# Performance work log

Hardware: AMD Instinct MI355X
Metric: run time of the kernel (lower is better)

## Reference

```python
import jax, jax.numpy as jnp
import numpy as np

K = 16  # k1: neighbors kept
D = 2   # d1: dilation


def setup_inputs() -> dict:
    key = jax.random.key(0)
    k1, k2 = jax.random.split(key)
    new_xyz = jax.random.normal(k1, (8, 4096, 3), dtype=jnp.float32)
    new_points = jax.random.normal(k2, (8, 4096, 64), dtype=jnp.float32)
    return {"new_xyz": new_xyz, "new_points": new_points}


def _dg_knn_idx(new_points):
    sq = jnp.sum(new_points * new_points, axis=-1)              # [B,N]
    inner = jnp.einsum('bnc,bmc->bnm', new_points, new_points)  # [B,N,N]
    adj = sq[:, :, None] - 2.0 * inner + sq[:, None, :]
    # dilated kNN: top (K*D) nearest, then stride by D
    _, idx = jax.lax.top_k(-adj, K * D)                         # [B,N,K*D]
    return idx[:, :, ::D]                                       # [B,N,K]


def reference(new_xyz, new_points):
    nn_idx = _dg_knn_idx(new_points)                            # [B,N,K] int32
    # index_points: gather neighbor coordinates -> [B,N,K,3]
    neighbor_xyz = jax.vmap(lambda pts, idx: pts[idx])(new_xyz, nn_idx)
    xyz_tile = jnp.broadcast_to(new_xyz[:, :, None, :], neighbor_xyz.shape)
    relative_xyz = xyz_tile - neighbor_xyz                      # [B,N,K,3]
    relative_dis = jnp.sqrt(jnp.sum(relative_xyz * relative_xyz, axis=-1, keepdims=True))
    # [B,N,K, 1+3+3+3] = [B,N,K,10]
    return jnp.concatenate([relative_dis, relative_xyz, xyz_tile, neighbor_xyz], axis=-1)
```

## Files before the change

### kernel.cpp

```cpp
#include <hip/hip_runtime.h>
#include <stdint.h>

typedef unsigned long long u64;
typedef __attribute__((ext_vector_type(8))) short s16x8;
typedef __attribute__((ext_vector_type(4))) float f32x4v;
typedef __attribute__((ext_vector_type(4))) unsigned int u32x4;
typedef __attribute__((ext_vector_type(2))) unsigned int u32x2;

#define NB 8
#define NPTS 4096
#define NC 64
#define KOUT 16
#define TSEL 48
#define CHUNK 64
#define NCHUNK (NPTS / CHUNK)
#define IDXBITS 0xFFFu
#define KEYMASK 0xFFFFF000u
#define RPW 4
#define RPB 16
#define ROWB 144

__global__ __launch_bounds__(256) void sq_kernel(const float* __restrict__ pts,
                                                 float* __restrict__ sqw) {
    int p = blockIdx.x * 256 + threadIdx.x;
    const float* r = pts + (size_t)p * NC;
    float acc[8];
#pragma unroll
    for (int j = 0; j < 8; ++j) acc[j] = __fmul_rn(r[j], r[j]);
#pragma unroll
    for (int i = 8; i < 64; i += 8)
#pragma unroll
        for (int j = 0; j < 8; ++j)
            acc[j] = __fadd_rn(acc[j], __fmul_rn(r[i + j], r[i + j]));
    float s01 = __fadd_rn(acc[0], acc[1]);
    float s23 = __fadd_rn(acc[2], acc[3]);
    float s45 = __fadd_rn(acc[4], acc[5]);
    float s67 = __fadd_rn(acc[6], acc[7]);
    sqw[p] = __fadd_rn(__fadd_rn(s01, s23), __fadd_rn(s45, s67));
}

static __device__ __forceinline__ uint32_t pkbf(float a, float b) {
#if __has_builtin(__builtin_amdgcn_perm)
    return __builtin_amdgcn_perm(__float_as_uint(b), __float_as_uint(a), 0x07060302);
#else
    return (__float_as_uint(b) & 0xFFFF0000u) | (__float_as_uint(a) >> 16);
#endif
}

__device__ __forceinline__ void stream_insert(uint32_t& list, uint32_t cand, int lane) {
    uint32_t thr = (uint32_t)__builtin_amdgcn_readlane((int)list, 47);
    u64 mask = __ballot(cand < thr);
    while (mask) {
        int src = __ffsll((long long)mask) - 1;
        uint32_t v = (uint32_t)__builtin_amdgcn_readlane((int)cand, src);
        int pos = __popcll(__ballot(list < v));
        uint32_t up = __shfl_up(list, 1);
        list = (lane < pos) ? list : ((lane == pos) ? v : up);
        mask &= (mask - 1);
    }
}

__device__ __forceinline__ void epilogue(uint32_t list, int n, int b, int lane,
                                         const float* __restrict__ pb,
                                         const float* __restrict__ sqb,
                                         float sqn,
                                         const float* __restrict__ xyz,
                                         float* __restrict__ out) {
    int m = (int)(list & IDXBITS);
    const float4* xr = (const float4*)(pb + (size_t)n * NC);
    const float4* yr = (const float4*)(pb + (size_t)m * NC);
    float acc = 0.f;
#pragma unroll
    for (int i = 0; i < 16; ++i) {
        float4 xv = xr[i];
        float4 yv = yr[i];
        acc = __fmaf_rn(xv.x, yv.x, acc);
        acc = __fmaf_rn(xv.y, yv.y, acc);
        acc = __fmaf_rn(xv.z, yv.z, acc);
        acc = __fmaf_rn(xv.w, yv.w, acc);
    }
    float key = __fadd_rn(__fsub_rn(sqn, __fmul_rn(2.0f, acc)), sqb[m]);

    int rank = 0;
    uint32_t kb = __float_as_uint(key);
#pragma unroll 1
    for (int j = 0; j < TSEL; ++j) {
        float kj = __uint_as_float(
            (uint32_t)__builtin_amdgcn_readlane((int)kb, j));
        int mj = __builtin_amdgcn_readlane(m, j);
        bool less = (kj < key) || (kj == key && mj < m);
        rank += less ? 1 : 0;
    }
    if (lane < TSEL && rank < 2 * KOUT && (rank & 1) == 0) {
        int k = rank >> 1;
        const float* xn = xyz + ((size_t)b * NPTS + n) * 3;
        const float* xm = xyz + ((size_t)b * NPTS + m) * 3;
        float xnx = xn[0], xny = xn[1], xnz = xn[2];
        float ox = xm[0], oy = xm[1], oz = xm[2];
        float rx = xnx - ox, ry = xny - oy, rz = xnz - oz;
        float dis = sqrtf(rx * rx + ry * ry + rz * rz);
        float* o = out + (((size_t)b * NPTS + n) * KOUT + k) * 10;
        o[0] = dis; o[1] = rx; o[2] = ry; o[3] = rz;
        o[4] = xnx; o[5] = xny; o[6] = xnz;
        o[7] = ox;  o[8] = oy;  o[9] = oz;
    }
}

__global__ __launch_bounds__(256, 3) void knn_kernel(
    const float* __restrict__ xyz,
    const float* __restrict__ pts,
    const float* __restrict__ sqw,
    float* __restrict__ out) {

    __shared__ __align__(16) unsigned short ylds[2][CHUNK * (ROWB / 2)];
    __shared__ __align__(16) float slds[4][16][20];

    const int tid = threadIdx.x;
    const int lane = tid & 63;
    const int wave = tid >> 6;
    const int b = blockIdx.x >> 8;
    const int rowbase = (blockIdx.x & 255) << 4;
    const int nw = __builtin_amdgcn_readfirstlane(rowbase + wave * RPW);
    const float* pb = pts + (size_t)b * NPTS * NC;
    const float* sqb = sqw + (size_t)b * NPTS;

    s16x8 afrag0, afrag1;
    {
        const float* xrow = pb + (size_t)(rowbase + (lane & 15)) * NC + (lane >> 4) * 8;
        float4 xa0 = *(const float4*)(xrow);
        float4 xa1 = *(const float4*)(xrow + 4);
        float4 xb0 = *(const float4*)(xrow + 32);
        float4 xb1 = *(const float4*)(xrow + 36);
        u32x4 a0p = { pkbf(xa0.x, xa0.y), pkbf(xa0.z, xa0.w),
                      pkbf(xa1.x, xa1.y), pkbf(xa1.z, xa1.w) };
        u32x4 a1p = { pkbf(xb0.x, xb0.y), pkbf(xb0.z, xb0.w),
                      pkbf(xb1.x, xb1.y), pkbf(xb1.z, xb1.w) };
        afrag0 = __builtin_bit_cast(s16x8, a0p);
        afrag1 = __builtin_bit_cast(s16x8, a1p);
    }

    const float sqn0 = sqb[nw + 0];
    const float sqn1 = sqb[nw + 1];
    const float sqn2 = sqb[nw + 2];
    const float sqn3 = sqb[nw + 3];

    uint32_t list0 = 0xFFFFFFFFu, list1 = 0xFFFFFFFFu;
    uint32_t list2 = 0xFFFFFFFFu, list3 = 0xFFFFFFFFu;

    const float4* gsrc = (const float4*)pb;
    float4 pf[4];
#pragma unroll
    for (int j = 0; j < 4; ++j) pf[j] = gsrc[tid + 256 * j];

#pragma unroll
    for (int j = 0; j < 4; ++j) {
        int s = tid + 256 * j;
        u32x2 w2 = { pkbf(pf[j].x, pf[j].y), pkbf(pf[j].z, pf[j].w) };
        *(u32x2*)((char*)ylds[0] + (s >> 4) * ROWB + (s & 15) * 8) = w2;
    }
    __syncthreads();

    for (int c = 0; c < NCHUNK; ++c) {
        const int cb = c & 1;
        if (c + 1 < NCHUNK) {
#pragma unroll
            for (int j = 0; j < 4; ++j)
                pf[j] = gsrc[(size_t)(c + 1) * (CHUNK * 16) + tid + 256 * j];
        }
        {
            const int m = c * CHUNK + lane;
            float sqm = sqb[m];
            const char* bp = (const char*)ylds[cb] + wave * (16 * ROWB)
                           + (lane & 15) * ROWB + (lane >> 4) * 16;
            s16x8 b0 = *(const s16x8*)(bp);
            s16x8 b1 = *(const s16x8*)(bp + 64);
            f32x4v cc = {0.f, 0.f, 0.f, 0.f};
            cc = __builtin_amdgcn_mfma_f32_16x16x32_bf16(afrag0, b0, cc, 0, 0, 0);
            cc = __builtin_amdgcn_mfma_f32_16x16x32_bf16(afrag1, b1, cc, 0, 0, 0);
            *(f32x4v*)&slds[wave][lane & 15][(lane >> 4) * 4] = cc;
            __syncthreads();
            f32x4v ip = *(const f32x4v*)&slds[lane >> 4][lane & 15][wave * 4];
            float t0 = fmaxf(fmaf(-2.f, ip.x, sqn0 + sqm), 0.f);
            float t1 = fmaxf(fmaf(-2.f, ip.y, sqn1 + sqm), 0.f);
            float t2 = fmaxf(fmaf(-2.f, ip.z, sqn2 + sqm), 0.f);
            float t3 = fmaxf(fmaf(-2.f, ip.w, sqn3 + sqm), 0.f);
            uint32_t c0 = (__float_as_uint(t0) & KEYMASK) | (unsigned)m;
            uint32_t c1 = (__float_as_uint(t1) & KEYMASK) | (unsigned)m;
            uint32_t c2 = (__float_as_uint(t2) & KEYMASK) | (unsigned)m;
            uint32_t c3 = (__float_as_uint(t3) & KEYMASK) | (unsigned)m;
            stream_insert(list0, c0, lane);
            stream_insert(list1, c1, lane);
            stream_insert(list2, c2, lane);
            stream_insert(list3, c3, lane);
        }
        if (c + 1 < NCHUNK) {
#pragma unroll
            for (int j = 0; j < 4; ++j) {
                int s = tid + 256 * j;
                u32x2 w2 = { pkbf(pf[j].x, pf[j].y), pkbf(pf[j].z, pf[j].w) };
                *(u32x2*)((char*)ylds[cb ^ 1] + (s >> 4) * ROWB + (s & 15) * 8) = w2;
            }
        }
        __syncthreads();
    }

    epilogue(list0, nw + 0, b, lane, pb, sqb, sqn0, xyz, out);
    epilogue(list1, nw + 1, b, lane, pb, sqb, sqn1, xyz, out);
    epilogue(list2, nw + 2, b, lane, pb, sqb, sqn2, xyz, out);
    epilogue(list3, nw + 3, b, lane, pb, sqb, sqn3, xyz, out);
}

extern "C" void kernel_launch(void* const* d_in, const int* in_sizes, int n_in,
                              void* d_out, int out_size, void* d_ws, size_t ws_size,
                              hipStream_t stream) {
    const float* xyz = (const float*)d_in[0];
    const float* pts = (const float*)d_in[1];
    float* sqw = (float*)d_ws;
    float* out = (float*)d_out;

    sq_kernel<<<(NB * NPTS) / 256, 256, 0, stream>>>(pts, sqw);
    knn_kernel<<<(NB * NPTS) / RPB, 256, 0, stream>>>(xyz, pts, sqw, out);
}
```

Before: 399.0 us.

## Process 32 query rows per block, 8 per wave, reusing each loaded chunk

Doubles the query rows handled per block from 16 to 32 (8 per wave). Each staged bf16 chunk of candidate points now feeds two MFMA tiles, which halves the redundant global loads and LDS staging per query row and halves the grid size. In exchange, each wave holds more register state (eight lists and more A fragments), the LDS transpose buffer grows, and the serial per-row insert work per wave doubles. This may lower occupancy and leave fewer blocks to spread across the compute units.

```diff
diff --git a/kernel.cpp b/kernel.cpp
--- a/kernel.cpp
+++ b/kernel.cpp
@@ -16,8 +16,8 @@
 #define NCHUNK (NPTS / CHUNK)
 #define IDXBITS 0xFFFu
 #define KEYMASK 0xFFFFF000u
-#define RPW 4
-#define RPB 16
+#define RPW 8
+#define RPB 32
 #define ROWB 144
 
 __global__ __launch_bounds__(256) void sq_kernel(const float* __restrict__ pts,
@@ -113,39 +113,44 @@
     float* __restrict__ out) {
 
     __shared__ __align__(16) unsigned short ylds[2][CHUNK * (ROWB / 2)];
-    __shared__ __align__(16) float slds[4][16][20];
+    __shared__ __align__(16) float slds[4][16][36];
 
     const int tid = threadIdx.x;
     const int lane = tid & 63;
     const int wave = tid >> 6;
-    const int b = blockIdx.x >> 8;
-    const int rowbase = (blockIdx.x & 255) << 4;
+    const int b = blockIdx.x >> 7;
+    const int rowbase = (blockIdx.x & 127) << 5;
     const int nw = __builtin_amdgcn_readfirstlane(rowbase + wave * RPW);
     const float* pb = pts + (size_t)b * NPTS * NC;
     const float* sqb = sqw + (size_t)b * NPTS;
 
-    s16x8 afrag0, afrag1;
+    s16x8 aA0, aA1, aB0, aB1;
     {
-        const float* xrow = pb + (size_t)(rowbase + (lane & 15)) * NC + (lane >> 4) * 8;
-        float4 xa0 = *(const float4*)(xrow);
-        float4 xa1 = *(const float4*)(xrow + 4);
-        float4 xb0 = *(const float4*)(xrow + 32);
-        float4 xb1 = *(const float4*)(xrow + 36);
-        u32x4 a0p = { pkbf(xa0.x, xa0.y), pkbf(xa0.z, xa0.w),
-                      pkbf(xa1.x, xa1.y), pkbf(xa1.z, xa1.w) };
-        u32x4 a1p = { pkbf(xb0.x, xb0.y), pkbf(xb0.z, xb0.w),
-                      pkbf(xb1.x, xb1.y), pkbf(xb1.z, xb1.w) };
-        afrag0 = __builtin_bit_cast(s16x8, a0p);
-        afrag1 = __builtin_bit_cast(s16x8, a1p);
-    }
-
-    const float sqn0 = sqb[nw + 0];
-    const float sqn1 = sqb[nw + 1];
-    const float sqn2 = sqb[nw + 2];
-    const float sqn3 = sqb[nw + 3];
-
-    uint32_t list0 = 0xFFFFFFFFu, list1 = 0xFFFFFFFFu;
-    uint32_t list2 = 0xFFFFFFFFu, list3 = 0xFFFFFFFFu;
+        const float* xrowA = pb + (size_t)(rowbase + (lane & 15)) * NC + (lane >> 4) * 8;
+        const float* xrowB = xrowA + 16 * NC;
+#pragma unroll
+        for (int h = 0; h < 2; ++h) {
+            const float* xr = h ? xrowB : xrowA;
+            float4 xa0 = *(const float4*)(xr);
+            float4 xa1 = *(const float4*)(xr + 4);
+            float4 xb0 = *(const float4*)(xr + 32);
+            float4 xb1 = *(const float4*)(xr + 36);
+            u32x4 p0 = { pkbf(xa0.x, xa0.y), pkbf(xa0.z, xa0.w),
+                         pkbf(xa1.x, xa1.y), pkbf(xa1.z, xa1.w) };
+            u32x4 p1 = { pkbf(xb0.x, xb0.y), pkbf(xb0.z, xb0.w),
+                         pkbf(xb1.x, xb1.y), pkbf(xb1.z, xb1.w) };
+            if (h == 0) { aA0 = __builtin_bit_cast(s16x8, p0); aA1 = __builtin_bit_cast(s16x8, p1); }
+            else        { aB0 = __builtin_bit_cast(s16x8, p0); aB1 = __builtin_bit_cast(s16x8, p1); }
+        }
+    }
+
+    float sqn[RPW];
+#pragma unroll
+    for (int r = 0; r < RPW; ++r) sqn[r] = sqb[nw + r];
+
+    uint32_t list[RPW];
+#pragma unroll
+    for (int r = 0; r < RPW; ++r) list[r] = 0xFFFFFFFFu;
 
     const float4* gsrc = (const float4*)pb;
     float4 pf[4];
@@ -174,24 +179,24 @@
                            + (lane & 15) * ROWB + (lane >> 4) * 16;
             s16x8 b0 = *(const s16x8*)(bp);
             s16x8 b1 = *(const s16x8*)(bp + 64);
-            f32x4v cc = {0.f, 0.f, 0.f, 0.f};
-            cc = __builtin_amdgcn_mfma_f32_16x16x32_bf16(afrag0, b0, cc, 0, 0, 0);
-            cc = __builtin_amdgcn_mfma_f32_16x16x32_bf16(afrag1, b1, cc, 0, 0, 0);
-            *(f32x4v*)&slds[wave][lane & 15][(lane >> 4) * 4] = cc;
+            f32x4v cc0 = {0.f, 0.f, 0.f, 0.f};
+            f32x4v cc1 = {0.f, 0.f, 0.f, 0.f};
+            cc0 = __builtin_amdgcn_mfma_f32_16x16x32_bf16(aA0, b0, cc0, 0, 0, 0);
+            cc0 = __builtin_amdgcn_mfma_f32_16x16x32_bf16(aA1, b1, cc0, 0, 0, 0);
+            cc1 = __builtin_amdgcn_mfma_f32_16x16x32_bf16(aB0, b0, cc1, 0, 0, 0);
+            cc1 = __builtin_amdgcn_mfma_f32_16x16x32_bf16(aB1, b1, cc1, 0, 0, 0);
+            *(f32x4v*)&slds[wave][lane & 15][(lane >> 4) * 4] = cc0;
+            *(f32x4v*)&slds[wave][lane & 15][16 + (lane >> 4) * 4] = cc1;
             __syncthreads();
-            f32x4v ip = *(const f32x4v*)&slds[lane >> 4][lane & 15][wave * 4];
-            float t0 = fmaxf(fmaf(-2.f, ip.x, sqn0 + sqm), 0.f);
-            float t1 = fmaxf(fmaf(-2.f, ip.y, sqn1 + sqm), 0.f);
-            float t2 = fmaxf(fmaf(-2.f, ip.z, sqn2 + sqm), 0.f);
-            float t3 = fmaxf(fmaf(-2.f, ip.w, sqn3 + sqm), 0.f);
-            uint32_t c0 = (__float_as_uint(t0) & KEYMASK) | (unsigned)m;
-            uint32_t c1 = (__float_as_uint(t1) & KEYMASK) | (unsigned)m;
-            uint32_t c2 = (__float_as_uint(t2) & KEYMASK) | (unsigned)m;
-            uint32_t c3 = (__float_as_uint(t3) & KEYMASK) | (unsigned)m;
-            stream_insert(list0, c0, lane);
-            stream_insert(list1, c1, lane);
-            stream_insert(list2, c2, lane);
-            stream_insert(list3, c3, lane);
+            f32x4v ipa = *(const f32x4v*)&slds[lane >> 4][lane & 15][wave * 8];
+            f32x4v ipb = *(const f32x4v*)&slds[lane >> 4][lane & 15][wave * 8 + 4];
+            float ip[RPW] = { ipa.x, ipa.y, ipa.z, ipa.w, ipb.x, ipb.y, ipb.z, ipb.w };
+#pragma unroll
+            for (int r = 0; r < RPW; ++r) {
+                float t = fmaxf(fmaf(-2.f, ip[r], sqn[r] + sqm), 0.f);
+                uint32_t cd = (__float_as_uint(t) & KEYMASK) | (unsigned)m;
+                stream_insert(list[r], cd, lane);
+            }
         }
         if (c + 1 < NCHUNK) {
 #pragma unroll
@@ -204,10 +209,9 @@
         __syncthreads();
     }
 
-    epilogue(list0, nw + 0, b, lane, pb, sqb, sqn0, xyz, out);
-    epilogue(list1, nw + 1, b, lane, pb, sqb, sqn1, xyz, out);
-    epilogue(list2, nw + 2, b, lane, pb, sqb, sqn2, xyz, out);
-    epilogue(list3, nw + 3, b, lane, pb, sqb, sqn3, xyz, out);
+#pragma unroll 1
+    for (int r = 0; r < RPW; ++r)
+        epilogue(list[r], nw + r, b, lane, pb, sqb, sqn[r], xyz, out);
 }
 
 extern "C" void kernel_launch(void* const* d_in, const int* in_sizes, int n_in,
```

Result: no change. 398.8 us (-0.1%).

## Double-buffer MFMA result scratch to drop one barrier per chunk; shrink candidate list

Applied to the files above, without the earlier changes.

The per-wave MFMA results now go into a double-buffered LDS scratch, so the transpose read and the stream insertion run after the existing end-of-chunk barrier. This removes the extra __syncthreads that sat in the middle of every chunk. The candidate list length TSEL also drops from 48 to 40, which lowers the insertion threshold and shortens the rank loop in the epilogue. The cost is that the 8-candidate margin for tie and bf16-approximation errors before exact re-ranking shrinks, which raises the risk of a wrong neighbour selection.

```diff
diff --git a/kernel.cpp b/kernel.cpp
--- a/kernel.cpp
+++ b/kernel.cpp
@@ -11,7 +11,7 @@
 #define NPTS 4096
 #define NC 64
 #define KOUT 16
-#define TSEL 48
+#define TSEL 40
 #define CHUNK 64
 #define NCHUNK (NPTS / CHUNK)
 #define IDXBITS 0xFFFu
@@ -48,7 +48,7 @@
 }
 
 __device__ __forceinline__ void stream_insert(uint32_t& list, uint32_t cand, int lane) {
-    uint32_t thr = (uint32_t)__builtin_amdgcn_readlane((int)list, 47);
+    uint32_t thr = (uint32_t)__builtin_amdgcn_readlane((int)list, TSEL - 1);
     u64 mask = __ballot(cand < thr);
     while (mask) {
         int src = __ffsll((long long)mask) - 1;
@@ -113,7 +113,7 @@
     float* __restrict__ out) {
 
     __shared__ __align__(16) unsigned short ylds[2][CHUNK * (ROWB / 2)];
-    __shared__ __align__(16) float slds[4][16][20];
+    __shared__ __align__(16) float slds[2][4][16][20];
 
     const int tid = threadIdx.x;
     const int lane = tid & 63;
@@ -139,13 +139,13 @@
         afrag1 = __builtin_bit_cast(s16x8, a1p);
     }
 
-    const float sqn0 = sqb[nw + 0];
-    const float sqn1 = sqb[nw + 1];
-    const float sqn2 = sqb[nw + 2];
-    const float sqn3 = sqb[nw + 3];
-
-    uint32_t list0 = 0xFFFFFFFFu, list1 = 0xFFFFFFFFu;
-    uint32_t list2 = 0xFFFFFFFFu, list3 = 0xFFFFFFFFu;
+    float sqn[RPW];
+#pragma unroll
+    for (int r = 0; r < RPW; ++r) sqn[r] = sqb[nw + r];
+
+    uint32_t list[RPW];
+#pragma unroll
+    for (int r = 0; r < RPW; ++r) list[r] = 0xFFFFFFFFu;
 
     const float4* gsrc = (const float4*)pb;
     float4 pf[4];
@@ -167,9 +167,9 @@
             for (int j = 0; j < 4; ++j)
                 pf[j] = gsrc[(size_t)(c + 1) * (CHUNK * 16) + tid + 256 * j];
         }
+        const int m = c * CHUNK + lane;
+        float sqm = sqb[m];
         {
-            const int m = c * CHUNK + lane;
-            float sqm = sqb[m];
             const char* bp = (const char*)ylds[cb] + wave * (16 * ROWB)
                            + (lane & 15) * ROWB + (lane >> 4) * 16;
             s16x8 b0 = *(const s16x8*)(bp);
@@ -177,21 +177,7 @@
             f32x4v cc = {0.f, 0.f, 0.f, 0.f};
             cc = __builtin_amdgcn_mfma_f32_16x16x32_bf16(afrag0, b0, cc, 0, 0, 0);
             cc = __builtin_amdgcn_mfma_f32_16x16x32_bf16(afrag1, b1, cc, 0, 0, 0);
-            *(f32x4v*)&slds[wave][lane & 15][(lane >> 4) * 4] = cc;
-            __syncthreads();
-            f32x4v ip = *(const f32x4v*)&slds[lane >> 4][lane & 15][wave * 4];
-            float t0 = fmaxf(fmaf(-2.f, ip.x, sqn0 + sqm), 0.f);
-            float t1 = fmaxf(fmaf(-2.f, ip.y, sqn1 + sqm), 0.f);
-            float t2 = fmaxf(fmaf(-2.f, ip.z, sqn2 + sqm), 0.f);
-            float t3 = fmaxf(fmaf(-2.f, ip.w, sqn3 + sqm), 0.f);
-            uint32_t c0 = (__float_as_uint(t0) & KEYMASK) | (unsigned)m;
-            uint32_t c1 = (__float_as_uint(t1) & KEYMASK) | (unsigned)m;
-            uint32_t c2 = (__float_as_uint(t2) & KEYMASK) | (unsigned)m;
-            uint32_t c3 = (__float_as_uint(t3) & KEYMASK) | (unsigned)m;
-            stream_insert(list0, c0, lane);
-            stream_insert(list1, c1, lane);
-            stream_insert(list2, c2, lane);
-            stream_insert(list3, c3, lane);
+            *(f32x4v*)&slds[cb][wave][lane & 15][(lane >> 4) * 4] = cc;
         }
         if (c + 1 < NCHUNK) {
 #pragma unroll
@@ -202,12 +188,21 @@
             }
         }
         __syncthreads();
-    }
-
-    epilogue(list0, nw + 0, b, lane, pb, sqb, sqn0, xyz, out);
-    epilogue(list1, nw + 1, b, lane, pb, sqb, sqn1, xyz, out);
-    epilogue(list2, nw + 2, b, lane, pb, sqb, sqn2, xyz, out);
-    epilogue(list3, nw + 3, b, lane, pb, sqb, sqn3, xyz, out);
+        {
+            f32x4v ip = *(const f32x4v*)&slds[cb][lane >> 4][lane & 15][wave * 4];
+            float ipr[RPW] = { ip.x, ip.y, ip.z, ip.w };
+#pragma unroll
+            for (int r = 0; r < RPW; ++r) {
+                float t = fmaxf(fmaf(-2.f, ipr[r], sqn[r] + sqm), 0.f);
+                uint32_t cd = (__float_as_uint(t) & KEYMASK) | (unsigned)m;
+                stream_insert(list[r], cd, lane);
+            }
+        }
+    }
+
+#pragma unroll 1
+    for (int r = 0; r < RPW; ++r)
+        epilogue(list[r], nw + r, b, lane, pb, sqb, sqn[r], xyz, out);
 }
 
 extern "C" void kernel_launch(void* const* d_in, const int* in_sizes, int n_in,
```

Result: faster. 365.1 us (-8.5%).
